# Performance work log

Hardware: AMD Instinct MI355X
Metric: run time of the kernel (lower is better)

The kernel has to match this reference:

```python
import jax, jax.numpy as jnp
import numpy as np

WS = 8           # window_size
NH = 8           # num_heads
VD = 384         # values_dim
CD = 128         # coords_dim
ID = 384         # inner_dim = inner_ratio * values_dim
HD = ID // NH    # head_dim = 48


def _rel_bias(pos_emb):
    # static Swin relative-position index table, gathers from pos_emb [2*WS-1, 2*WS-1]
    idx = np.array([[x, y] for x in range(WS) for y in range(WS)])
    rel = idx[None, :, :] - idx[:, None, :] + WS - 1  # [64,64,2]
    return pos_emb[rel[:, :, 0], rel[:, :, 1]]        # [64,64]


def _rmsnorm(x, w, eps=1e-6):
    return x * jax.lax.rsqrt(jnp.mean(x * x, axis=-1, keepdims=True) + eps) * w


def _to_windows(t):
    # t: [b, Hp, Wp, D] with feature layout (e H) -> [b, NH, Wh, Ww, WS*WS, e]
    b, Hp, Wp, D = t.shape
    e = D // NH
    t = t.reshape(b, Hp // WS, WS, Wp // WS, WS, e, NH)
    t = t.transpose(0, 6, 1, 3, 2, 4, 5)
    return t.reshape(b, NH, Hp // WS, Wp // WS, WS * WS, e)


def setup_inputs() -> dict:
    key = jax.random.key(0)
    ks = jax.random.split(key, 8)
    B, H, W = 2, 192, 192
    s = 0.02
    return {
        "values": jax.random.normal(ks[0], (B, H, W, VD), jnp.float32),
        "coords": jax.random.normal(ks[1], (B, H, W, CD), jnp.float32),
        "W_vqk": jax.random.normal(ks[2], (VD, 2 * ID), jnp.float32) * s,
        "b_vqk": jnp.zeros((2 * ID,), jnp.float32),
        "g_vqk": jnp.ones((2 * ID,), jnp.float32),
        "W_vv": jax.random.normal(ks[3], (VD, ID), jnp.float32) * s,
        "b_vv": jnp.zeros((ID,), jnp.float32),
        "W_cqk": jax.random.normal(ks[4], (CD, 2 * ID), jnp.float32) * s,
        "b_cqk": jnp.zeros((2 * ID,), jnp.float32),
        "g_cqk": jnp.ones((2 * ID,), jnp.float32),
        "att_lambda": jax.random.normal(ks[5], (1,), jnp.float32),
        "pos_emb": jax.random.normal(ks[6], (2 * WS - 1, 2 * WS - 1), jnp.float32),
        "W_ov": jax.random.normal(ks[7], (ID, VD), jnp.float32) * s,
        "b_ov": jnp.zeros((VD,), jnp.float32),
    }


def reference(values, coords, W_vqk, b_vqk, g_vqk, W_vv, b_vv,
              W_cqk, b_cqk, g_cqk, att_lambda, pos_emb, W_ov, b_ov):
    b, h, w, _ = values.shape  # h, w divisible by WS -> torch F.pad would add 0
    # values path: cat([RMSNorm(Linear_qk(x)), Linear_v(x)]); '(d k)' with k=3
    # means q/k/v are INTERLEAVED along the feature dim (index d*3+k).
    vqk = _rmsnorm(values @ W_vqk + b_vqk, g_vqk)            # [b,h,w,2*ID]
    vv_ = values @ W_vv + b_vv                               # [b,h,w,ID]
    vcat = jnp.concatenate([vqk, vv_], axis=-1).reshape(b, h, w, ID, 3)
    qv, kv, vv = vcat[..., 0], vcat[..., 1], vcat[..., 2]
    # coords path (update_coords=False): interleaved split k=2
    cqk = _rmsnorm(coords @ W_cqk + b_cqk, g_cqk).reshape(b, h, w, ID, 2)
    qc, kc = cqk[..., 0], cqk[..., 1]
    # shifted=True: roll by -WS//2 (NOTE: original never rolls back)
    shift = -(WS // 2)
    roll = lambda t: jnp.roll(t, (shift, shift), axis=(1, 2))
    qv, kv, vv, qc, kc = (_to_windows(roll(t)) for t in (qv, kv, vv, qc, kc))
    # fused value+coord scores with learned lambda
    dots = (jnp.einsum('bHxyie,bHxyje->bHxyij', qv, kv)
            + att_lambda[0] * jnp.einsum('bHxyie,bHxyje->bHxyij', qc, kc)) / np.sqrt(HD)
    dots = dots + _rel_bias(pos_emb)
    # shifted-window masks on last window row / last window column
    s = WS * (WS // 2)
    n = WS * WS
    row_mask = jnp.zeros((n, n), jnp.float32)
    row_mask = row_mask.at[-s:, :-s].set(-jnp.inf).at[:-s, -s:].set(-jnp.inf)
    col_mask = row_mask.reshape(WS, WS, WS, WS).transpose(1, 0, 3, 2).reshape(n, n)
    dots = dots.at[:, :, -1, :].add(row_mask)
    dots = dots.at[:, :, :, -1].add(col_mask)
    att = jax.nn.softmax(dots, axis=-1)
    yv = jnp.einsum('bHxyij,bHxyje->bHxyie', att, vv)  # [b,NH,Wh,Ww,64,HD]
    Wh, Ww = h // WS, w // WS
    # output layout '(H e)' -> heads slow, e fast
    yv = yv.reshape(b, NH, Wh, Ww, WS, WS, HD).transpose(0, 2, 4, 3, 5, 1, 6)
    yv = yv.reshape(b, Wh * WS, Ww * WS, ID)[:, :h, :w, :]
    return yv @ W_ov + b_ov
```

## Files before the change

kernel.cpp:

```cpp
#include <hip/hip_runtime.h>
#include <hip/hip_bf16.h>

typedef __hip_bfloat16 bf16;
typedef __attribute__((ext_vector_type(8))) short bf16x8;
typedef __attribute__((ext_vector_type(4))) short bf16x4;
typedef __attribute__((ext_vector_type(4))) float f32x4;

#define CPIX 12288

__device__ __forceinline__ float tof(bf16 x){ return __bfloat162float(x); }
__device__ __forceinline__ bf16  tob(float x){ return __float2bfloat16(x); }
__device__ __forceinline__ float bf2f(short s){ return __uint_as_float(((unsigned)(unsigned short)s) << 16); }

__global__ __launch_bounds__(256) void wprep_k(
    const float* __restrict__ W_vqk, const float* __restrict__ W_vv, const float* __restrict__ W_cqk,
    const float* __restrict__ W_ov,  const float* __restrict__ b_vqk, const float* __restrict__ b_vv,
    const float* __restrict__ b_cqk, const float* __restrict__ g_vqk, const float* __restrict__ g_cqk,
    bf16* __restrict__ W1Tp, bf16* __restrict__ WcTp, bf16* __restrict__ WoT,
    float* __restrict__ bP0, float* __restrict__ bPc, float* __restrict__ gvP, float* __restrict__ gcP)
{
  int idx = blockIdx.x*256 + threadIdx.x;
  if (idx < 442368) {
    int n = idx/384, k = idx - n*384;
    int role = n/384, rem = n - role*384, h = rem/48, e = rem - (rem/48)*48;
    int c = 24*e + 3*h + role;
    float v = (e < 32) ? W_vqk[k*768 + c] : W_vv[k*384 + (c - 768)];
    W1Tp[n*384 + k] = tob(v);
  } else if (idx < 540672) {
    int q = idx - 442368;
    int n = q >> 7, k = q & 127;
    int role = n/384, rem = n - role*384, h = rem/48, e = rem - (rem/48)*48;
    WcTp[n*128 + k] = tob(W_cqk[k*768 + 16*e + 2*h + role]);
  } else if (idx < 688128) {
    int q = idx - 540672;
    int n = q/384, k = q - n*384;
    WoT[n*384 + k] = tob(W_ov[k*384 + n]);
  } else if (idx < 689280) {
    int n = idx - 688128;
    int role = n/384, rem = n - role*384, h = rem/48, e = rem - (rem/48)*48;
    int c = 24*e + 3*h + role;
    bP0[n] = (e < 32) ? b_vqk[c] : b_vv[c - 768];
  } else if (idx < 690048) {
    int n = idx - 689280;
    int role = n/384, rem = n - role*384, h = rem/48, e = rem - (rem/48)*48;
    bPc[n] = b_cqk[16*e + 2*h + role];
  } else if (idx < 691200) {
    int n = idx - 690048;
    int role = n/384, rem = n - role*384, h = rem/48, e = rem - (rem/48)*48;
    gvP[n] = (e < 32) ? g_vqk[24*e + 3*h + role] : 1.0f;
  } else if (idx < 691968) {
    int n = idx - 691200;
    int role = n/384, rem = n - role*384, h = rem/48, e = rem - (rem/48)*48;
    gcP[n] = g_cqk[16*e + 2*h + role];
  }
}

__global__ __launch_bounds__(256) void prep_k(const float* __restrict__ vals, const float* __restrict__ crds,
                                              bf16* __restrict__ Vb, bf16* __restrict__ Cb,
                                              float* __restrict__ rms_v, float* __restrict__ rms_c,
                                              int bb, int hf)
{
  int u = blockIdx.x*256 + threadIdx.x;
  if (u < CPIX) rms_v[u] = 0.f;
  else if (u < 2*CPIX) rms_c[u - CPIX] = 0.f;
  int pix, c8;
  const float* src; bf16* dst;
  if (u < 589824) { pix = u/48; c8 = u - pix*48; }
  else { int u2 = u - 589824; pix = u2 >> 4; c8 = u2 & 15; }
  int lr = pix/192, lc = pix - (pix/192)*192;
  int srow = (hf*64 + lr + 4) % 192;
  int scol = (lc + 4) % 192;
  if (u < 589824) { src = vals + (((size_t)bb*192 + srow)*192 + scol)*384 + c8*8; dst = Vb + (size_t)pix*384 + c8*8; }
  else            { src = crds + (((size_t)bb*192 + srow)*192 + scol)*128 + c8*8; dst = Cb + (size_t)pix*128 + c8*8; }
  float4 f0 = *(const float4*)src;
  float4 f1 = *(const float4*)(src + 4);
  union { bf16 h[8]; uint4 u4; } t;
  t.h[0]=tob(f0.x); t.h[1]=tob(f0.y); t.h[2]=tob(f0.z); t.h[3]=tob(f0.w);
  t.h[4]=tob(f1.x); t.h[5]=tob(f1.y); t.h[6]=tob(f1.z); t.h[7]=tob(f1.w);
  *(uint4*)dst = t.u4;
}

template<int MODE>
__global__ __launch_bounds__(256,4) void gemm_k(const bf16* __restrict__ A, const bf16* __restrict__ WT,
    const float* __restrict__ biasP, bf16* __restrict__ outb, float* __restrict__ outf,
    float* __restrict__ rsum, int pix0)
{
  constexpr int KTOT = (MODE==1) ? 128 : 384;
  constexpr int NT   = (MODE==0) ? 1152 : (MODE==1) ? 768 : 384;
  constexpr int BM   = (MODE==2) ? 64 : 128;
  constexpr int MT4  = BM/32;
  constexpr int ACH  = BM*8;
  __shared__ bf16 As[BM][72];
  __shared__ bf16 Bs[128][72];
  const int tid = threadIdx.x, lane = tid & 63, wid = tid >> 6;
  const int wr = (wid >> 1)*(BM/2), wc = (wid & 1)*64;
  const int rowbase = blockIdx.x*BM;
  const int nbase   = blockIdx.y*128;

  f32x4 acc[MT4][4] = {};
  for (int ks = 0; ks < KTOT; ks += 64) {
    __syncthreads();
    #pragma unroll
    for (int it = 0; it < (ACH + 1024)/256; it++) {
      int idx = it*256 + tid;
      if (idx < ACH) {
        int r = idx >> 3, c = idx & 7;
        *(uint4*)&As[r][c*8] = *(const uint4*)(A + (size_t)(rowbase + r)*KTOT + ks + c*8);
      } else {
        int q = idx - ACH; int r = q >> 3, c = q & 7;
        *(uint4*)&Bs[r][c*8] = *(const uint4*)(WT + (size_t)(nbase + r)*KTOT + ks + c*8);
      }
    }
    __syncthreads();
    #pragma unroll
    for (int k2 = 0; k2 < 64; k2 += 32) {
      const int kb = k2 + (lane >> 4)*8, ml = lane & 15;
      bf16x8 a[MT4], b[4];
      #pragma unroll
      for (int t = 0; t < MT4; t++) a[t] = *(const bf16x8*)&As[wr + t*16 + ml][kb];
      #pragma unroll
      for (int t = 0; t < 4; t++)  b[t] = *(const bf16x8*)&Bs[wc + t*16 + ml][kb];
      #pragma unroll
      for (int mt = 0; mt < MT4; mt++)
      #pragma unroll
      for (int nt = 0; nt < 4; nt++)
        acc[mt][nt] = __builtin_amdgcn_mfma_f32_16x16x32_bf16(a[mt], b[nt], acc[mt][nt], 0, 0, 0);
    }
  }
  const int lr4 = (lane >> 4)*4, lcol = lane & 15;
  #pragma unroll
  for (int mt = 0; mt < MT4; mt++) {
    #pragma unroll
    for (int i = 0; i < 4; i++) {
      int pix = rowbase + wr + mt*16 + lr4 + i;
      float sq_ = 0.f;
      #pragma unroll
      for (int nt = 0; nt < 4; nt++) {
        int n = nbase + wc + nt*16 + lcol;
        float v = acc[mt][nt][i] + biasP[n];
        if constexpr (MODE == 2) {
          outf[(size_t)(pix0 + pix)*384 + n] = v;
        } else {
          outb[(size_t)pix*NT + n] = tob(v);
          if (MODE == 1 || (n % 48) < 32) sq_ += v*v;
        }
      }
      if constexpr (MODE != 2) {
        sq_ += __shfl_xor(sq_, 1); sq_ += __shfl_xor(sq_, 2);
        sq_ += __shfl_xor(sq_, 4); sq_ += __shfl_xor(sq_, 8);
        if (lcol == 0) atomicAdd(&rsum[pix], sq_);
      }
    }
  }
}

__global__ __launch_bounds__(256) void finish_k(float* __restrict__ rms_v, float* __restrict__ rms_c)
{
  int i = blockIdx.x*256 + threadIdx.x;
  if (i < CPIX) rms_v[i] = rsqrtf(rms_v[i]*(1.f/768.f) + 1e-6f);
  else if (i < 2*CPIX) { int j = i - CPIX; rms_c[j] = rsqrtf(rms_c[j]*(1.f/768.f) + 1e-6f); }
}

__device__ __forceinline__ bf16x8 pack8g(uint4 raw, float r, float4 ga, float4 gb)
{
  union { uint4 u4; unsigned short us[8]; } rw; rw.u4 = raw;
  union { bf16x8 v; bf16 h[8]; } o;
  o.h[0] = tob(bf2f((short)rw.us[0]) * (r * ga.x));
  o.h[1] = tob(bf2f((short)rw.us[1]) * (r * ga.y));
  o.h[2] = tob(bf2f((short)rw.us[2]) * (r * ga.z));
  o.h[3] = tob(bf2f((short)rw.us[3]) * (r * ga.w));
  o.h[4] = tob(bf2f((short)rw.us[4]) * (r * gb.x));
  o.h[5] = tob(bf2f((short)rw.us[5]) * (r * gb.y));
  o.h[6] = tob(bf2f((short)rw.us[6]) * (r * gb.z));
  o.h[7] = tob(bf2f((short)rw.us[7]) * (r * gb.w));
  return o.v;
}

__global__ __launch_bounds__(256,4) void attn_k(const bf16* __restrict__ Y0, const bf16* __restrict__ Yc,
    const float* __restrict__ rms_v, const float* __restrict__ rms_c,
    const float* __restrict__ gvP, const float* __restrict__ gcP,
    const float* __restrict__ lam_p, const float* __restrict__ pos,
    bf16* __restrict__ y_att, int hf)
{
  __shared__ bf16 Ks[64][104];
  __shared__ bf16 Vt[48][72];
  __shared__ bf16 Pb[64][72];
  __shared__ float sq[96];
  __shared__ float poss[225];
  const int tid = threadIdx.x, lane = tid & 63, w = tid >> 6;
  const int win = blockIdx.x, h = blockIdx.y;
  const int wx = win/24, wy = win - (win/24)*24;
  const float lam = lam_p[0];
  const float SCL = 0.14433756729740643f;

  if (tid < 96) sq[tid] = (tid < 48 ? gvP[h*48 + tid] : gcP[h*48 + tid - 48]*lam) * SCL;
  if (tid < 225) poss[tid] = pos[tid];

  {
    const int j = lane;
    const int p = (wx*8 + (j>>3))*192 + wy*8 + (j&7);
    const float rvj = rms_v[p], rcj = rms_c[p];
    for (int grp = w; grp < 18; grp += 4) {
      if (grp < 6) {
        int c = grp;
        uint4 raw = *(const uint4*)(Y0 + (size_t)p*1152 + 384 + h*48 + c*8);
        const float* gp = gvP + 384 + h*48 + c*8;
        float4 ga = *(const float4*)gp, gb = *(const float4*)(gp+4);
        float r = (c < 4) ? rvj : 1.0f;
        union { bf16x8 v; uint4 u4; } o; o.v = pack8g(raw, r, ga, gb);
        *(uint4*)&Ks[j][c*8] = o.u4;
      } else if (grp < 12) {
        int c = grp - 6;
        uint4 raw = *(const uint4*)(Yc + (size_t)p*768 + 384 + h*48 + c*8);
        const float* gp = gcP + 384 + h*48 + c*8;
        float4 ga = *(const float4*)gp, gb = *(const float4*)(gp+4);
        union { bf16x8 v; uint4 u4; } o; o.v = pack8g(raw, rcj, ga, gb);
        *(uint4*)&Ks[j][48 + c*8] = o.u4;
      } else {
        int c = grp - 12;
        uint4 raw = *(const uint4*)(Y0 + (size_t)p*1152 + 768 + h*48 + c*8);
        const float* gp = gvP + 768 + h*48 + c*8;
        float4 ga = *(const float4*)gp, gb = *(const float4*)(gp+4);
        float r = (c < 4) ? rvj : 1.0f;
        union { uint4 u4; unsigned short us[8]; } rw; rw.u4 = raw;
        Vt[c*8+0][j] = tob(bf2f((short)rw.us[0]) * (r * ga.x));
        Vt[c*8+1][j] = tob(bf2f((short)rw.us[1]) * (r * ga.y));
        Vt[c*8+2][j] = tob(bf2f((short)rw.us[2]) * (r * ga.z));
        Vt[c*8+3][j] = tob(bf2f((short)rw.us[3]) * (r * ga.w));
        Vt[c*8+4][j] = tob(bf2f((short)rw.us[4]) * (r * gb.x));
        Vt[c*8+5][j] = tob(bf2f((short)rw.us[5]) * (r * gb.y));
        Vt[c*8+6][j] = tob(bf2f((short)rw.us[6]) * (r * gb.z));
        Vt[c*8+7][j] = tob(bf2f((short)rw.us[7]) * (r * gb.w));
      }
    }
  }
  __syncthreads();

  const int ml = lane & 15, k0 = (lane >> 4)*8;
  const int mrow = w*16 + ml;
  const int pA = (wx*8 + (mrow>>3))*192 + wy*8 + (mrow&7);
  const float rvA = rms_v[pA], rcA = rms_c[pA];
  bf16x8 qf0, qf1, qf2;
  {
    uint4 r0 = *(const uint4*)(Y0 + (size_t)pA*1152 + h*48 + k0);
    float4 ga = *(const float4*)&sq[k0],      gb = *(const float4*)&sq[k0+4];
    qf0 = pack8g(r0, rvA, ga, gb);
    const bf16* s1 = (k0 < 16) ? (Y0 + (size_t)pA*1152 + h*48 + 32 + k0)
                               : (Yc + (size_t)pA*768  + h*48 + (k0 - 16));
    float r1 = (k0 < 16) ? 1.0f : rcA;
    uint4 raw1 = *(const uint4*)s1;
    ga = *(const float4*)&sq[32+k0]; gb = *(const float4*)&sq[36+k0];
    qf1 = pack8g(raw1, r1, ga, gb);
    uint4 r2 = *(const uint4*)(Yc + (size_t)pA*768 + h*48 + 16 + k0);
    ga = *(const float4*)&sq[64+k0]; gb = *(const float4*)&sq[68+k0];
    qf2 = pack8g(r2, rcA, ga, gb);
  }

  f32x4 acc[4] = {};
  #pragma unroll
  for (int nt = 0; nt < 4; nt++) {
    bf16x8 b0 = *(const bf16x8*)&Ks[nt*16 + ml][k0];
    bf16x8 b1 = *(const bf16x8*)&Ks[nt*16 + ml][32 + k0];
    bf16x8 b2 = *(const bf16x8*)&Ks[nt*16 + ml][64 + k0];
    acc[nt] = __builtin_amdgcn_mfma_f32_16x16x32_bf16(qf0, b0, acc[nt], 0, 0, 0);
    acc[nt] = __builtin_amdgcn_mfma_f32_16x16x32_bf16(qf1, b1, acc[nt], 0, 0, 0);
    acc[nt] = __builtin_amdgcn_mfma_f32_16x16x32_bf16(qf2, b2, acc[nt], 0, 0, 0);
  }

  const bool rowm = (hf == 2) && (wx == 7);
  const bool colm = (wy == 23);
  const int g4 = (lane >> 4)*4;
  float pv[4][4];
  float inv_[4];
  #pragma unroll
  for (int i = 0; i < 4; i++) {
    int r = w*16 + g4 + i;
    int txi = r >> 3, tyi = r & 7;
    #pragma unroll
    for (int nt = 0; nt < 4; nt++) {
      int j = nt*16 + ml;
      int txj = j >> 3, tyj = j & 7;
      float v = acc[nt][i] + poss[(txj - txi + 7)*15 + (tyj - tyi + 7)];
      if ((rowm && ((txi >= 4) != (txj >= 4))) || (colm && ((tyi >= 4) != (tyj >= 4)))) v = -1e30f;
      pv[i][nt] = v;
    }
    float mx = fmaxf(fmaxf(pv[i][0], pv[i][1]), fmaxf(pv[i][2], pv[i][3]));
    #pragma unroll
    for (int m = 1; m < 16; m <<= 1) mx = fmaxf(mx, __shfl_xor(mx, m));
    float s0 = 0.f;
    #pragma unroll
    for (int nt = 0; nt < 4; nt++) { pv[i][nt] = __expf(pv[i][nt] - mx); s0 += pv[i][nt]; }
    #pragma unroll
    for (int m = 1; m < 16; m <<= 1) s0 += __shfl_xor(s0, m);
    inv_[i] = 1.f / s0;
  }
  #pragma unroll
  for (int i = 0; i < 4; i++)
  #pragma unroll
  for (int nt = 0; nt < 4; nt++)
    Pb[w*16 + g4 + i][nt*16 + ml] = tob(pv[i][nt]);

  f32x4 o0 = {}, o1 = {}, o2 = {};
  {
    bf16x8 a0 = *(const bf16x8*)&Pb[w*16 + ml][k0];
    bf16x8 b;
    b = *(const bf16x8*)&Vt[ 0 + ml][k0];      o0 = __builtin_amdgcn_mfma_f32_16x16x32_bf16(a0, b, o0, 0, 0, 0);
    b = *(const bf16x8*)&Vt[16 + ml][k0];      o1 = __builtin_amdgcn_mfma_f32_16x16x32_bf16(a0, b, o1, 0, 0, 0);
    b = *(const bf16x8*)&Vt[32 + ml][k0];      o2 = __builtin_amdgcn_mfma_f32_16x16x32_bf16(a0, b, o2, 0, 0, 0);
    bf16x8 a1 = *(const bf16x8*)&Pb[w*16 + ml][32 + k0];
    b = *(const bf16x8*)&Vt[ 0 + ml][32 + k0]; o0 = __builtin_amdgcn_mfma_f32_16x16x32_bf16(a1, b, o0, 0, 0, 0);
    b = *(const bf16x8*)&Vt[16 + ml][32 + k0]; o1 = __builtin_amdgcn_mfma_f32_16x16x32_bf16(a1, b, o1, 0, 0, 0);
    b = *(const bf16x8*)&Vt[32 + ml][32 + k0]; o2 = __builtin_amdgcn_mfma_f32_16x16x32_bf16(a1, b, o2, 0, 0, 0);
  }

  #pragma unroll
  for (int i = 0; i < 4; i++) {
    Pb[w*16 + g4 + i][     ml] = tob(o0[i] * inv_[i]);
    Pb[w*16 + g4 + i][16 + ml] = tob(o1[i] * inv_[i]);
    Pb[w*16 + g4 + i][32 + ml] = tob(o2[i] * inv_[i]);
  }
  #pragma unroll
  for (int s2 = 0; s2 < 3; s2++) {
    int u = s2*64 + lane;
    int row = u / 12, seg = u - row*12;
    int rr = w*16 + row;
    int pC = (wx*8 + (rr>>3))*192 + wy*8 + (rr&7);
    uint2 d = *(const uint2*)&Pb[rr][seg*4];
    *(uint2*)(y_att + (size_t)pC*384 + h*48 + seg*4) = d;
  }
}

extern "C" void kernel_launch(void* const* d_in, const int* in_sizes, int n_in,
                              void* d_out, int out_size, void* d_ws, size_t ws_size,
                              hipStream_t stream)
{
  const float* values = (const float*)d_in[0];
  const float* coords = (const float*)d_in[1];
  const float* W_vqk  = (const float*)d_in[2];
  const float* b_vqk  = (const float*)d_in[3];
  const float* g_vqk  = (const float*)d_in[4];
  const float* W_vv   = (const float*)d_in[5];
  const float* b_vv   = (const float*)d_in[6];
  const float* W_cqk  = (const float*)d_in[7];
  const float* b_cqk  = (const float*)d_in[8];
  const float* g_cqk  = (const float*)d_in[9];
  const float* lam    = (const float*)d_in[10];
  const float* pos    = (const float*)d_in[11];
  const float* W_ov   = (const float*)d_in[12];
  const float* b_ov   = (const float*)d_in[13];
  float* out = (float*)d_out;

  char* ws = (char*)d_ws;
  bf16*  W1Tp  = (bf16*)(ws + 0);
  bf16*  WcTp  = (bf16*)(ws + 884736);
  bf16*  WoT   = (bf16*)(ws + 1081344);
  float* bP0   = (float*)(ws + 1376256);
  float* bPc   = (float*)(ws + 1380864);
  float* gvP   = (float*)(ws + 1383936);
  float* gcP   = (float*)(ws + 1388544);
  bf16*  Vb    = (bf16*)(ws + 1391616);
  bf16*  Cb    = (bf16*)(ws + 10828800);
  bf16*  Y0    = (bf16*)(ws + 13974528);
  bf16*  Yc    = (bf16*)(ws + 42286080);
  float* rms_v = (float*)(ws + 61160448);
  float* rms_c = (float*)(ws + 61209600);
  bf16*  y_att = (bf16*)(ws + 61258752);
  (void)ws_size; (void)in_sizes; (void)n_in; (void)out_size;

  wprep_k<<<2703, 256, 0, stream>>>(W_vqk, W_vv, W_cqk, W_ov, b_vqk, b_vv, b_cqk, g_vqk, g_cqk,
                                    W1Tp, WcTp, WoT, bP0, bPc, gvP, gcP);

  for (int ch = 0; ch < 6; ch++) {
    int bb = ch/3, hf = ch - bb*3;
    prep_k<<<3072, 256, 0, stream>>>(values, coords, Vb, Cb, rms_v, rms_c, bb, hf);
    gemm_k<0><<<dim3(96,9), 256, 0, stream>>>(Vb, W1Tp, bP0, Y0, nullptr, rms_v, 0);
    gemm_k<1><<<dim3(96,6), 256, 0, stream>>>(Cb, WcTp, bPc, Yc, nullptr, rms_c, 0);
    finish_k<<<96, 256, 0, stream>>>(rms_v, rms_c);
    attn_k<<<dim3(192,8), 256, 0, stream>>>(Y0, Yc, rms_v, rms_c, gvP, gcP, lam, pos, y_att, hf);
    gemm_k<2><<<dim3(192,3), 256, 0, stream>>>(y_att, WoT, b_ov, nullptr, out, nullptr, ch*CPIX);
  }
}
```

Measured before the change: 702.6 us.

## Fuse fp32 input conversion and roll into projection GEMM loads, drop prep/finish kernels

Removes the prep kernel that converted values/coords to rolled bf16 buffers and instead has the projection GEMMs read fp32 inputs directly with the shifted-row index, converting to bf16 while staging into shared memory. The RMS finalize kernel is removed and the rsqrt is computed inside the attention kernel. The sum-of-squares buffers are zeroed in the output GEMM for the next chunk, with the first chunk's zeroing done in the weight prep kernel. This cuts launches and an intermediate bf16 round trip, at the cost of GEMM tile loads reading twice the bytes (fp32), recomputing the roll indices, and re-reading fp32 A across each column block.

```diff
diff --git a/kernel.cpp b/kernel.cpp
--- a/kernel.cpp
+++ b/kernel.cpp
@@ -3,7 +3,6 @@
 
 typedef __hip_bfloat16 bf16;
 typedef __attribute__((ext_vector_type(8))) short bf16x8;
-typedef __attribute__((ext_vector_type(4))) short bf16x4;
 typedef __attribute__((ext_vector_type(4))) float f32x4;
 
 #define CPIX 12288
@@ -17,7 +16,8 @@
     const float* __restrict__ W_ov,  const float* __restrict__ b_vqk, const float* __restrict__ b_vv,
     const float* __restrict__ b_cqk, const float* __restrict__ g_vqk, const float* __restrict__ g_cqk,
     bf16* __restrict__ W1Tp, bf16* __restrict__ WcTp, bf16* __restrict__ WoT,
-    float* __restrict__ bP0, float* __restrict__ bPc, float* __restrict__ gvP, float* __restrict__ gcP)
+    float* __restrict__ bP0, float* __restrict__ bPc, float* __restrict__ gvP, float* __restrict__ gcP,
+    float* __restrict__ rs_v, float* __restrict__ rs_c)
 {
   int idx = blockIdx.x*256 + threadIdx.x;
   if (idx < 442368) {
@@ -52,38 +52,17 @@
     int n = idx - 691200;
     int role = n/384, rem = n - role*384, h = rem/48, e = rem - (rem/48)*48;
     gcP[n] = g_cqk[16*e + 2*h + role];
-  }
-}
-
-__global__ __launch_bounds__(256) void prep_k(const float* __restrict__ vals, const float* __restrict__ crds,
-                                              bf16* __restrict__ Vb, bf16* __restrict__ Cb,
-                                              float* __restrict__ rms_v, float* __restrict__ rms_c,
-                                              int bb, int hf)
-{
-  int u = blockIdx.x*256 + threadIdx.x;
-  if (u < CPIX) rms_v[u] = 0.f;
-  else if (u < 2*CPIX) rms_c[u - CPIX] = 0.f;
-  int pix, c8;
-  const float* src; bf16* dst;
-  if (u < 589824) { pix = u/48; c8 = u - pix*48; }
-  else { int u2 = u - 589824; pix = u2 >> 4; c8 = u2 & 15; }
-  int lr = pix/192, lc = pix - (pix/192)*192;
-  int srow = (hf*64 + lr + 4) % 192;
-  int scol = (lc + 4) % 192;
-  if (u < 589824) { src = vals + (((size_t)bb*192 + srow)*192 + scol)*384 + c8*8; dst = Vb + (size_t)pix*384 + c8*8; }
-  else            { src = crds + (((size_t)bb*192 + srow)*192 + scol)*128 + c8*8; dst = Cb + (size_t)pix*128 + c8*8; }
-  float4 f0 = *(const float4*)src;
-  float4 f1 = *(const float4*)(src + 4);
-  union { bf16 h[8]; uint4 u4; } t;
-  t.h[0]=tob(f0.x); t.h[1]=tob(f0.y); t.h[2]=tob(f0.z); t.h[3]=tob(f0.w);
-  t.h[4]=tob(f1.x); t.h[5]=tob(f1.y); t.h[6]=tob(f1.z); t.h[7]=tob(f1.w);
-  *(uint4*)dst = t.u4;
+  } else if (idx < 716544) {
+    int q = idx - 691968;
+    if (q < CPIX) rs_v[q] = 0.f; else rs_c[q - CPIX] = 0.f;
+  }
 }
 
 template<int MODE>
-__global__ __launch_bounds__(256,4) void gemm_k(const bf16* __restrict__ A, const bf16* __restrict__ WT,
-    const float* __restrict__ biasP, bf16* __restrict__ outb, float* __restrict__ outf,
-    float* __restrict__ rsum, int pix0)
+__global__ __launch_bounds__(256,4) void gemm_k(const float* __restrict__ Af, const bf16* __restrict__ Ab,
+    const bf16* __restrict__ WT, const float* __restrict__ biasP,
+    bf16* __restrict__ outb, float* __restrict__ outf, float* __restrict__ rsum,
+    float* __restrict__ z0, float* __restrict__ z1, int bb, int hf, int pix0)
 {
   constexpr int KTOT = (MODE==1) ? 128 : 384;
   constexpr int NT   = (MODE==0) ? 1152 : (MODE==1) ? 768 : 384;
@@ -97,6 +76,13 @@
   const int rowbase = blockIdx.x*BM;
   const int nbase   = blockIdx.y*128;
 
+  if constexpr (MODE == 2) {
+    if (blockIdx.y == 0) {
+      if (tid < 64) z0[rowbase + tid] = 0.f;
+      else if (tid < 128) z1[rowbase + tid - 64] = 0.f;
+    }
+  }
+
   f32x4 acc[MT4][4] = {};
   for (int ks = 0; ks < KTOT; ks += 64) {
     __syncthreads();
@@ -105,7 +91,21 @@
       int idx = it*256 + tid;
       if (idx < ACH) {
         int r = idx >> 3, c = idx & 7;
-        *(uint4*)&As[r][c*8] = *(const uint4*)(A + (size_t)(rowbase + r)*KTOT + ks + c*8);
+        if constexpr (MODE == 2) {
+          *(uint4*)&As[r][c*8] = *(const uint4*)(Ab + (size_t)(rowbase + r)*KTOT + ks + c*8);
+        } else {
+          int pix = rowbase + r;
+          int lr = pix/192, lc = pix - (pix/192)*192;
+          int srow = (hf*64 + lr + 4) % 192;
+          int scol = (lc + 4) % 192;
+          const float* src = Af + (((size_t)bb*192 + srow)*192 + scol)*KTOT + ks + c*8;
+          float4 f0 = *(const float4*)src;
+          float4 f1 = *(const float4*)(src + 4);
+          union { bf16 h[8]; uint4 u4; } t;
+          t.h[0]=tob(f0.x); t.h[1]=tob(f0.y); t.h[2]=tob(f0.z); t.h[3]=tob(f0.w);
+          t.h[4]=tob(f1.x); t.h[5]=tob(f1.y); t.h[6]=tob(f1.z); t.h[7]=tob(f1.w);
+          *(uint4*)&As[r][c*8] = t.u4;
+        }
       } else {
         int q = idx - ACH; int r = q >> 3, c = q & 7;
         *(uint4*)&Bs[r][c*8] = *(const uint4*)(WT + (size_t)(nbase + r)*KTOT + ks + c*8);
@@ -154,13 +154,6 @@
   }
 }
 
-__global__ __launch_bounds__(256) void finish_k(float* __restrict__ rms_v, float* __restrict__ rms_c)
-{
-  int i = blockIdx.x*256 + threadIdx.x;
-  if (i < CPIX) rms_v[i] = rsqrtf(rms_v[i]*(1.f/768.f) + 1e-6f);
-  else if (i < 2*CPIX) { int j = i - CPIX; rms_c[j] = rsqrtf(rms_c[j]*(1.f/768.f) + 1e-6f); }
-}
-
 __device__ __forceinline__ bf16x8 pack8g(uint4 raw, float r, float4 ga, float4 gb)
 {
   union { uint4 u4; unsigned short us[8]; } rw; rw.u4 = raw;
@@ -176,8 +169,10 @@
   return o.v;
 }
 
+__device__ __forceinline__ float rmsf(float s){ return rsqrtf(s*(1.f/768.f) + 1e-6f); }
+
 __global__ __launch_bounds__(256,4) void attn_k(const bf16* __restrict__ Y0, const bf16* __restrict__ Yc,
-    const float* __restrict__ rms_v, const float* __restrict__ rms_c,
+    const float* __restrict__ rs_v, const float* __restrict__ rs_c,
     const float* __restrict__ gvP, const float* __restrict__ gcP,
     const float* __restrict__ lam_p, const float* __restrict__ pos,
     bf16* __restrict__ y_att, int hf)
@@ -199,7 +194,7 @@
   {
     const int j = lane;
     const int p = (wx*8 + (j>>3))*192 + wy*8 + (j&7);
-    const float rvj = rms_v[p], rcj = rms_c[p];
+    const float rvj = rmsf(rs_v[p]), rcj = rmsf(rs_c[p]);
     for (int grp = w; grp < 18; grp += 4) {
       if (grp < 6) {
         int c = grp;
@@ -239,7 +234,7 @@
   const int ml = lane & 15, k0 = (lane >> 4)*8;
   const int mrow = w*16 + ml;
   const int pA = (wx*8 + (mrow>>3))*192 + wy*8 + (mrow&7);
-  const float rvA = rms_v[pA], rcA = rms_c[pA];
+  const float rvA = rmsf(rs_v[pA]), rcA = rmsf(rs_c[pA]);
   bf16x8 qf0, qf1, qf2;
   {
     uint4 r0 = *(const uint4*)(Y0 + (size_t)pA*1152 + h*48 + k0);
@@ -358,25 +353,24 @@
   float* bPc   = (float*)(ws + 1380864);
   float* gvP   = (float*)(ws + 1383936);
   float* gcP   = (float*)(ws + 1388544);
-  bf16*  Vb    = (bf16*)(ws + 1391616);
-  bf16*  Cb    = (bf16*)(ws + 10828800);
-  bf16*  Y0    = (bf16*)(ws + 13974528);
-  bf16*  Yc    = (bf16*)(ws + 42286080);
-  float* rms_v = (float*)(ws + 61160448);
-  float* rms_c = (float*)(ws + 61209600);
-  bf16*  y_att = (bf16*)(ws + 61258752);
+  bf16*  Y0    = (bf16*)(ws + 1391616);
+  bf16*  Yc    = (bf16*)(ws + 29703168);
+  float* rs_v  = (float*)(ws + 48577536);
+  float* rs_c  = (float*)(ws + 48626688);
+  bf16*  y_att = (bf16*)(ws + 48675840);
   (void)ws_size; (void)in_sizes; (void)n_in; (void)out_size;
 
-  wprep_k<<<2703, 256, 0, stream>>>(W_vqk, W_vv, W_cqk, W_ov, b_vqk, b_vv, b_cqk, g_vqk, g_cqk,
-                                    W1Tp, WcTp, WoT, bP0, bPc, gvP, gcP);
+  wprep_k<<<2799, 256, 0, stream>>>(W_vqk, W_vv, W_cqk, W_ov, b_vqk, b_vv, b_cqk, g_vqk, g_cqk,
+                                    W1Tp, WcTp, WoT, bP0, bPc, gvP, gcP, rs_v, rs_c);
 
   for (int ch = 0; ch < 6; ch++) {
     int bb = ch/3, hf = ch - bb*3;
-    prep_k<<<3072, 256, 0, stream>>>(values, coords, Vb, Cb, rms_v, rms_c, bb, hf);
-    gemm_k<0><<<dim3(96,9), 256, 0, stream>>>(Vb, W1Tp, bP0, Y0, nullptr, rms_v, 0);
-    gemm_k<1><<<dim3(96,6), 256, 0, stream>>>(Cb, WcTp, bPc, Yc, nullptr, rms_c, 0);
-    finish_k<<<96, 256, 0, stream>>>(rms_v, rms_c);
-    attn_k<<<dim3(192,8), 256, 0, stream>>>(Y0, Yc, rms_v, rms_c, gvP, gcP, lam, pos, y_att, hf);
-    gemm_k<2><<<dim3(192,3), 256, 0, stream>>>(y_att, WoT, b_ov, nullptr, out, nullptr, ch*CPIX);
-  }
-}
+    gemm_k<0><<<dim3(96,9), 256, 0, stream>>>(values, nullptr, W1Tp, bP0, Y0, nullptr, rs_v,
+                                              nullptr, nullptr, bb, hf, 0);
+    gemm_k<1><<<dim3(96,6), 256, 0, stream>>>(coords, nullptr, WcTp, bPc, Yc, nullptr, rs_c,
+                                              nullptr, nullptr, bb, hf, 0);
+    attn_k<<<dim3(192,8), 256, 0, stream>>>(Y0, Yc, rs_v, rs_c, gvP, gcP, lam, pos, y_att, hf);
+    gemm_k<2><<<dim3(192,3), 256, 0, stream>>>(nullptr, y_att, WoT, b_ov, nullptr, out, nullptr,
+                                               rs_v, rs_c, 0, 0, ch*CPIX);
+  }
+}
```

Result: no change. 696.9 us (-0.8%).
